# Kernel tuning notes

Hardware: AMD Instinct MI355X
Metric: run time of the kernel (lower is better)

## Reference

```python
import jax, jax.numpy as jnp
import numpy as np

CONF_THRESHOLD = 0.25
IOU_THRESHOLD = 0.5
MAX_OUT_DETS = 300
CELL_DIM = 640.0
PRE_NMS_TOPK = 4096  # fixed-size candidate set for jit-compatible NMS
N_ANCHORS = 134400   # 2560px input, strides 8/16/32
N_CLASSES = 80


def setup_inputs() -> dict:
    key = jax.random.key(0)
    preds = jax.random.uniform(key, (1, 4 + N_CLASSES, N_ANCHORS), dtype=jnp.float32)
    # scale the 4 box channels (xc, yc, w, h) to pixel range, keep class scores in [0,1]
    scale = jnp.concatenate([jnp.full((4,), CELL_DIM, jnp.float32),
                             jnp.ones((N_CLASSES,), jnp.float32)])
    preds = preds * scale[None, :, None]
    return {"yolo_preds": preds}


def _pairwise_iou(boxes):
    # boxes: [K, 4] in x1,y1,x2,y2 — torchvision-style IoU (no +1)
    area = (boxes[:, 2] - boxes[:, 0]) * (boxes[:, 3] - boxes[:, 1])
    lt = jnp.maximum(boxes[:, None, :2], boxes[None, :, :2])
    rb = jnp.minimum(boxes[:, None, 2:], boxes[None, :, 2:])
    wh = jnp.clip(rb - lt, 0.0)
    inter = wh[..., 0] * wh[..., 1]
    union = area[:, None] + area[None, :] - inter
    return inter / (union + 1e-9)


def _forward(yolo_preds):
    p = yolo_preds[0]                      # [4+C, A] (batch index [0] as in original)
    cls = p[4:4 + N_CLASSES]               # [C, A]
    scores = jnp.max(cls, axis=0)          # [A]
    classes = jnp.argmax(cls, axis=0)      # [A] int

    # box decode: note torch float `//` is floor division
    xc, yc, w, h = p[0], p[1], p[2], p[3]
    hw = jnp.floor(w / 2.0)
    hh = jnp.floor(h / 2.0)
    boxes = jnp.stack([xc - hw, yc - hh, xc + hw, yc + hh], axis=1)  # [A, 4]

    # confidence threshold mask (jit-compatible: mask to -inf instead of dynamic filter)
    masked = jnp.where(scores >= CONF_THRESHOLD, scores, -jnp.inf)

    # fixed-size pre-NMS top-k candidate selection (sorted descending)
    cand_scores, idx = jax.lax.top_k(masked, PRE_NMS_TOPK)   # [K]
    cand_boxes = boxes[idx]                                   # [K, 4]
    cand_classes = classes[idx]                               # [K]
    cand_valid = jnp.isfinite(cand_scores)                    # padding / below-threshold

    # greedy class-agnostic NMS (original uses plain torchvision.ops.nms)
    iou = _pairwise_iou(cand_boxes)                           # [K, K]
    k_idx = jnp.arange(PRE_NMS_TOPK)
    suppress = (iou > IOU_THRESHOLD) & (k_idx[None, :] > k_idx[:, None])  # j>i upper tri

    def body(i, keep):
        sup = suppress[i] & keep[i]
        return keep & ~sup

    keep = jax.lax.fori_loop(0, PRE_NMS_TOPK, body, cand_valid)

    # final top-k among survivors
    kept_scores = jnp.where(keep, cand_scores, -jnp.inf)
    final_scores, fidx = jax.lax.top_k(kept_scores, MAX_OUT_DETS)
    final_valid = jnp.isfinite(final_scores)
    final_boxes = jnp.where(final_valid[:, None], cand_boxes[fidx] / CELL_DIM, 0.0)
    final_classes = jnp.where(final_valid, cand_classes[fidx], 0)
    final_scores = jnp.where(final_valid, final_scores, 0.0)

    # tie-break quirk from the original: if the last two scores are ~equal,
    # zero out every score within 1e-5 of the last one
    tie = jnp.abs(final_scores[-1] - final_scores[-2]) < 1e-6
    factor = jnp.where(tie,
                       (final_scores - final_scores[-1] > 1e-5).astype(final_scores.dtype),
                       jnp.ones((), final_scores.dtype))
    final_scores = final_scores * factor

    count = jnp.sum(final_scores > 1e-5)
    return final_boxes, final_scores, final_classes, count


def reference(yolo_preds):
    return _forward(yolo_preds)
```

## Files before the change

kernel.cpp:

```cpp
#include <hip/hip_runtime.h>
#include <math.h>

#define N_ANCH 134400
#define N_CLS  80
#define TOPK   4096
#define MAX_OUT 300
#define TIECAP 16384

#define SARR_OFF   0u
#define GHIST_OFF  537600u
#define STATE_OFF  541696u
#define CNT_OFF    541704u
#define TIECNT_OFF 541708u
#define CLS8_OFF   541712u
#define TIEBUF_OFF 676112u
#define CANDK_OFF  741648u
#define CBOX_OFF   774416u
#define CSCORE_OFF 839952u
#define CCLS_OFF   856336u
#define SUP_OFF    872720u
#define WS_NEEDED  2969872u
#define MEMSET_OFF 537600u
#define MEMSET_LEN 4112u

static __device__ __forceinline__ unsigned int ord_f32(float f) {
  unsigned int u = __float_as_uint(f);
  return (u & 0x80000000u) ? ~u : (u | 0x80000000u);
}
static __device__ __forceinline__ float unord_f32(unsigned int o) {
  unsigned int u = (o & 0x80000000u) ? (o ^ 0x80000000u) : ~o;
  return __uint_as_float(u);
}

__global__ __launch_bounds__(256) void k_keys(const float* __restrict__ p,
                                              unsigned int* __restrict__ sarr,
                                              unsigned char* __restrict__ cls8,
                                              unsigned int* __restrict__ ghist) {
  __shared__ unsigned int h[256];
  int tid = threadIdx.x;
  h[tid] = 0u;
  __syncthreads();
  int i = blockIdx.x * 256 + tid;
  float best = p[4 * N_ANCH + i];
  int cls = 0;
  for (int c = 1; c < N_CLS; ++c) {
    float v = p[(4 + c) * N_ANCH + i];
    if (v > best) { best = v; cls = c; }
  }
  float m = (best >= 0.25f) ? best : -INFINITY;
  unsigned int s = ord_f32(m);
  sarr[i] = s;
  cls8[i] = (unsigned char)cls;
  atomicAdd(&h[s >> 24], 1u);
  __syncthreads();
  if (h[tid]) atomicAdd(&ghist[tid], h[tid]);
}

template <int PASS>
__global__ __launch_bounds__(256) void k_hist(const unsigned int* __restrict__ sarr,
                                              const unsigned int* __restrict__ state,
                                              unsigned int* __restrict__ ghist) {
  __shared__ unsigned int h[256];
  int tid = threadIdx.x;
  h[tid] = 0u;
  __syncthreads();
  int i = blockIdx.x * 256 + tid;
  unsigned int s = sarr[i];
  const int sh = 24 - 8 * PASS;
  if ((s >> (sh + 8)) == state[0])
    atomicAdd(&h[(s >> sh) & 255u], 1u);
  __syncthreads();
  if (h[tid]) atomicAdd(&ghist[PASS * 256 + tid], h[tid]);
}

template <int PASS>
__global__ __launch_bounds__(256) void k_scan(const unsigned int* __restrict__ ghist,
                                              unsigned int* __restrict__ state) {
  __shared__ unsigned int h[256];
  int tid = threadIdx.x;
  h[tid] = ghist[PASS * 256 + tid];
  __syncthreads();
  if (tid == 0) {
    unsigned int r    = (PASS == 0) ? (unsigned)TOPK : state[1];
    unsigned int pref = (PASS == 0) ? 0u : state[0];
    unsigned int cum = 0u;
    for (int b = 255; b >= 0; --b) {
      unsigned int c = h[b];
      if (cum + c >= r) { state[0] = (pref << 8) | (unsigned int)b; state[1] = r - cum; break; }
      cum += c;
    }
  }
}

__global__ void k_gathertie(const unsigned int* __restrict__ sarr,
                            const unsigned int* __restrict__ state,
                            unsigned int* __restrict__ counter,
                            unsigned int* __restrict__ tiecnt,
                            unsigned int* __restrict__ tiebuf,
                            unsigned long long* __restrict__ candk) {
  int i = blockIdx.x * 256 + threadIdx.x;
  unsigned int s = sarr[i];
  unsigned int S = state[0];
  if (s > S) {
    unsigned int pos = atomicAdd(counter, 1u);
    if (pos < TOPK)
      candk[pos] = ((unsigned long long)s << 32) |
                   (unsigned long long)(~(unsigned int)i);
  } else if (s == S) {
    unsigned int tp = atomicAdd(tiecnt, 1u);
    if (tp < TIECAP) tiebuf[tp] = (unsigned int)i;
  }
}

__global__ __launch_bounds__(256) void k_tieappend(const unsigned int* __restrict__ state,
                                                   const unsigned int* __restrict__ counter,
                                                   const unsigned int* __restrict__ tiecnt,
                                                   const unsigned int* __restrict__ tiebuf,
                                                   unsigned long long* __restrict__ candk) {
  __shared__ unsigned int buf[TIECAP];
  unsigned int n = *tiecnt; if (n > TIECAP) n = TIECAP;
  unsigned int rf = state[1];
  unsigned int cnt0 = *counter;
  unsigned long long Shi = ((unsigned long long)state[0]) << 32;
  for (unsigned int t = threadIdx.x; t < n; t += 256) buf[t] = tiebuf[t];
  __syncthreads();
  for (unsigned int t = threadIdx.x; t < n; t += 256) {
    unsigned int v = buf[t], r = 0u;
    for (unsigned int j = 0; j < n; ++j) r += (buf[j] < v) ? 1u : 0u;
    if (r < rf) candk[cnt0 + r] = Shi | (unsigned long long)(~v);
  }
}

__global__ __launch_bounds__(1024) void k_sort(unsigned long long* __restrict__ candk) {
  __shared__ unsigned long long s[TOPK];
  for (int i = threadIdx.x; i < TOPK; i += 1024) s[i] = candk[i];
  __syncthreads();
  for (int k = 2; k <= TOPK; k <<= 1) {
    for (int j = k >> 1; j > 0; j >>= 1) {
      for (int i = threadIdx.x; i < TOPK; i += 1024) {
        int ixj = i ^ j;
        if (ixj > i) {
          bool up = ((i & k) == 0);
          unsigned long long a = s[i], b = s[ixj];
          bool sw = up ? (a < b) : (a > b);
          if (sw) { s[i] = b; s[ixj] = a; }
        }
      }
      __syncthreads();
    }
  }
  for (int i = threadIdx.x; i < TOPK; i += 1024) candk[i] = s[i];
}

__global__ void k_fill(const float* __restrict__ p,
                       const unsigned char* __restrict__ cls8,
                       const unsigned long long* __restrict__ candk,
                       float4* __restrict__ cbox,
                       float* __restrict__ cscore,
                       int* __restrict__ ccls) {
  int c = blockIdx.x * blockDim.x + threadIdx.x;
  if (c >= TOPK) return;
  unsigned long long k = candk[c];
  float score = unord_f32((unsigned int)(k >> 32));
  int idx = (int)(~(unsigned int)(k & 0xFFFFFFFFull));
  float xc = p[idx];
  float yc = p[N_ANCH + idx];
  float w  = p[2 * N_ANCH + idx];
  float h  = p[3 * N_ANCH + idx];
  float hw = floorf(w * 0.5f), hh = floorf(h * 0.5f);
  cbox[c] = make_float4(xc - hw, yc - hh, xc + hw, yc + hh);
  cscore[c] = score;
  ccls[c]   = (int)cls8[idx];
}

__global__ void k_iou(const float4* __restrict__ cbox, unsigned long long* __restrict__ sup) {
  int g = blockIdx.x * blockDim.x + threadIdx.x;
  int row = g >> 6, word = g & 63;
  float4 bi = cbox[row];
  float ai = (bi.z - bi.x) * (bi.w - bi.y);
  unsigned long long m = 0ull;
  int j0 = word << 6;
  if (j0 + 63 > row) {
    for (int b = 0; b < 64; ++b) {
      int j = j0 + b;
      if (j <= row) continue;
      float4 bj = cbox[j];
      float aj = (bj.z - bj.x) * (bj.w - bj.y);
      float ltx = fmaxf(bi.x, bj.x), lty = fmaxf(bi.y, bj.y);
      float rbx = fminf(bi.z, bj.z), rby = fminf(bi.w, bj.w);
      float ww = fmaxf(rbx - ltx, 0.0f), hh = fmaxf(rby - lty, 0.0f);
      float inter = ww * hh;
      float uni = ai + aj - inter;
      float iou = inter / (uni + 1e-9f);
      if (iou > 0.5f) m |= (1ull << b);
    }
  }
  sup[g] = m;
}

__global__ __launch_bounds__(256) void k_nms_out(const float4* __restrict__ cbox,
                                                 const float* __restrict__ cscore,
                                                 const int* __restrict__ ccls,
                                                 const unsigned long long* __restrict__ sup,
                                                 float* __restrict__ out) {
  __shared__ unsigned long long skeep[64];
  __shared__ unsigned long long s_keptl;
  __shared__ int s_list[MAX_OUT];
  __shared__ float s_fs[MAX_OUT];
  __shared__ int s_K;
  __shared__ int s_cnt;
  int tid = threadIdx.x;
  int lane = tid & 63, wave = tid >> 6;

  for (int r = 0; r < 16; ++r) {
    float sc = cscore[r * 256 + tid];
    unsigned long long m = __ballot(sc >= 0.25f);
    if (lane == 0) skeep[r * 4 + wave] = m;
  }
  if (tid == 0) { s_K = 0; s_cnt = 0; }
  __syncthreads();

  for (int chunk = 0; chunk < 64; ++chunk) {
    unsigned long long cur0 = skeep[chunk];
    if (cur0 == 0ull) continue;
    unsigned long long rowv[16];
#pragma unroll
    for (int t = 0; t < 16; ++t)
      rowv[t] = sup[(unsigned)(chunk * 64 + wave * 16 + t) * 64 + lane];
    if (wave == 0) {
      unsigned long long diag = sup[(chunk * 64 + lane) * 64 + chunk];
      unsigned long long cur = cur0;
      unsigned long long keptl = 0ull;
      int n = s_K;
      while (cur) {
        int b = __builtin_ctzll(cur);
        if (lane == 0) s_list[n] = chunk * 64 + b;
        n++;
        keptl |= (1ull << b);
        if (n == MAX_OUT) break;
        unsigned long long mb = __shfl(diag, b);
        cur &= ~mb;
        cur = (b == 63) ? 0ull : (cur & (~0ull << (b + 1)));
      }
      if (lane == 0) { s_K = n; s_keptl = keptl; }
    }
    __syncthreads();
    if (s_K >= MAX_OUT) break;
    unsigned long long keptl = s_keptl;
    unsigned long long acc = 0ull;
#pragma unroll
    for (int t = 0; t < 16; ++t) {
      unsigned long long sel = 0ull - ((keptl >> (wave * 16 + t)) & 1ull);
      acc |= rowv[t] & sel;
    }
    if (acc) atomicAnd(&skeep[lane], ~acc);
    __syncthreads();
  }
  __syncthreads();

  int K = s_K;
  for (int r = tid; r < MAX_OUT; r += 256)
    s_fs[r] = (r < K) ? cscore[s_list[r]] : 0.0f;
  __syncthreads();

  float slast = s_fs[MAX_OUT - 1], sprev = s_fs[MAX_OUT - 2];
  bool tie = fabsf(slast - sprev) < 1e-6f;
  int local = 0;
  for (int r = tid; r < MAX_OUT; r += 256) {
    float fs = s_fs[r];
    float factor = tie ? ((fs - slast > 1e-5f) ? 1.0f : 0.0f) : 1.0f;
    float so = fs * factor;
    out[4 * MAX_OUT + r] = so;
    if (so > 1e-5f) local++;
    if (r < K) {
      int c = s_list[r];
      float4 b = cbox[c];
      out[4 * r + 0] = b.x / 640.0f;
      out[4 * r + 1] = b.y / 640.0f;
      out[4 * r + 2] = b.z / 640.0f;
      out[4 * r + 3] = b.w / 640.0f;
      out[5 * MAX_OUT + r] = (float)ccls[c];
    } else {
      out[4 * r + 0] = 0.0f; out[4 * r + 1] = 0.0f;
      out[4 * r + 2] = 0.0f; out[4 * r + 3] = 0.0f;
      out[5 * MAX_OUT + r] = 0.0f;
    }
  }
  if (local) atomicAdd(&s_cnt, local);
  __syncthreads();
  if (tid == 0) out[6 * MAX_OUT] = (float)s_cnt;
}

extern "C" void kernel_launch(void* const* d_in, const int* in_sizes, int n_in,
                              void* d_out, int out_size, void* d_ws, size_t ws_size,
                              hipStream_t stream) {
  const float* p = (const float*)d_in[0];
  float* out = (float*)d_out;
  char* ws = (char*)d_ws;

  if (ws_size < (size_t)WS_NEEDED) return;

  unsigned int* sarr    = (unsigned int*)(ws + SARR_OFF);
  unsigned int* ghist   = (unsigned int*)(ws + GHIST_OFF);
  unsigned int* state   = (unsigned int*)(ws + STATE_OFF);
  unsigned int* counter = (unsigned int*)(ws + CNT_OFF);
  unsigned int* tiecnt  = (unsigned int*)(ws + TIECNT_OFF);
  unsigned char* cls8   = (unsigned char*)(ws + CLS8_OFF);
  unsigned int* tiebuf  = (unsigned int*)(ws + TIEBUF_OFF);
  unsigned long long* candk = (unsigned long long*)(ws + CANDK_OFF);
  float4* cbox              = (float4*)(ws + CBOX_OFF);
  float* cscore             = (float*)(ws + CSCORE_OFF);
  int* ccls                 = (int*)(ws + CCLS_OFF);
  unsigned long long* sup   = (unsigned long long*)(ws + SUP_OFF);

  const int NB = N_ANCH / 256;

  hipMemsetAsync(ws + MEMSET_OFF, 0, MEMSET_LEN, stream);
  k_keys<<<NB, 256, 0, stream>>>(p, sarr, cls8, ghist);
  k_scan<0><<<1, 256, 0, stream>>>(ghist, state);
  k_hist<1><<<NB, 256, 0, stream>>>(sarr, state, ghist);
  k_scan<1><<<1, 256, 0, stream>>>(ghist, state);
  k_hist<2><<<NB, 256, 0, stream>>>(sarr, state, ghist);
  k_scan<2><<<1, 256, 0, stream>>>(ghist, state);
  k_hist<3><<<NB, 256, 0, stream>>>(sarr, state, ghist);
  k_scan<3><<<1, 256, 0, stream>>>(ghist, state);
  k_gathertie<<<NB, 256, 0, stream>>>(sarr, state, counter, tiecnt, tiebuf, candk);
  k_tieappend<<<1, 256, 0, stream>>>(state, counter, tiecnt, tiebuf, candk);
  k_sort<<<1, 1024, 0, stream>>>(candk);
  k_fill<<<TOPK / 256, 256, 0, stream>>>(p, cls8, candk, cbox, cscore, ccls);
  k_iou<<<(TOPK * 64) / 256, 256, 0, stream>>>(cbox, sup);
  k_nms_out<<<1, 256, 0, stream>>>(cbox, cscore, ccls, sup, out);
}
```

Baseline: 310.2 us.

## Replace single-block bitonic sort with parallel rank-counting scatter fused into fill

Removes the one-block bitonic sort of the 4096 candidate keys and the separate fill kernel. A new kernel runs across 16 blocks. Each block loads all keys into shared memory, each thread counts how many keys are larger than its own to get its sorted rank, then decodes the box and scatters it to that rank. This swaps the serial-latency sort with many barriers for O(K^2) parallel comparisons spread over more CUs, and saves one launch. It relies on the keys being unique (the index is in the low bits) so the ranks form a permutation.

```diff
diff --git a/kernel.cpp b/kernel.cpp
--- a/kernel.cpp
+++ b/kernel.cpp
@@ -131,46 +131,31 @@
   }
 }
 
-__global__ __launch_bounds__(1024) void k_sort(unsigned long long* __restrict__ candk) {
-  __shared__ unsigned long long s[TOPK];
-  for (int i = threadIdx.x; i < TOPK; i += 1024) s[i] = candk[i];
-  __syncthreads();
-  for (int k = 2; k <= TOPK; k <<= 1) {
-    for (int j = k >> 1; j > 0; j >>= 1) {
-      for (int i = threadIdx.x; i < TOPK; i += 1024) {
-        int ixj = i ^ j;
-        if (ixj > i) {
-          bool up = ((i & k) == 0);
-          unsigned long long a = s[i], b = s[ixj];
-          bool sw = up ? (a < b) : (a > b);
-          if (sw) { s[i] = b; s[ixj] = a; }
-        }
-      }
-      __syncthreads();
-    }
-  }
-  for (int i = threadIdx.x; i < TOPK; i += 1024) candk[i] = s[i];
-}
-
-__global__ void k_fill(const float* __restrict__ p,
-                       const unsigned char* __restrict__ cls8,
-                       const unsigned long long* __restrict__ candk,
-                       float4* __restrict__ cbox,
-                       float* __restrict__ cscore,
-                       int* __restrict__ ccls) {
-  int c = blockIdx.x * blockDim.x + threadIdx.x;
-  if (c >= TOPK) return;
-  unsigned long long k = candk[c];
-  float score = unord_f32((unsigned int)(k >> 32));
-  int idx = (int)(~(unsigned int)(k & 0xFFFFFFFFull));
+__global__ __launch_bounds__(256) void k_rankfill(const float* __restrict__ p,
+                                                  const unsigned char* __restrict__ cls8,
+                                                  const unsigned long long* __restrict__ candk,
+                                                  float4* __restrict__ cbox,
+                                                  float* __restrict__ cscore,
+                                                  int* __restrict__ ccls) {
+  __shared__ unsigned long long keys[TOPK];
+  int tid = threadIdx.x;
+  for (int i = tid; i < TOPK; i += 256) keys[i] = candk[i];
+  __syncthreads();
+  int c = blockIdx.x * 256 + tid;
+  unsigned long long mine = keys[c];
+  int cnt = 0;
+#pragma unroll 8
+  for (int j = 0; j < TOPK; ++j) cnt += (keys[j] > mine) ? 1 : 0;
+  float score = unord_f32((unsigned int)(mine >> 32));
+  int idx = (int)(~(unsigned int)(mine & 0xFFFFFFFFull));
   float xc = p[idx];
   float yc = p[N_ANCH + idx];
   float w  = p[2 * N_ANCH + idx];
   float h  = p[3 * N_ANCH + idx];
   float hw = floorf(w * 0.5f), hh = floorf(h * 0.5f);
-  cbox[c] = make_float4(xc - hw, yc - hh, xc + hw, yc + hh);
-  cscore[c] = score;
-  ccls[c]   = (int)cls8[idx];
+  cbox[cnt] = make_float4(xc - hw, yc - hh, xc + hw, yc + hh);
+  cscore[cnt] = score;
+  ccls[cnt]   = (int)cls8[idx];
 }
 
 __global__ void k_iou(const float4* __restrict__ cbox, unsigned long long* __restrict__ sup) {
@@ -326,8 +311,7 @@
   k_scan<3><<<1, 256, 0, stream>>>(ghist, state);
   k_gathertie<<<NB, 256, 0, stream>>>(sarr, state, counter, tiecnt, tiebuf, candk);
   k_tieappend<<<1, 256, 0, stream>>>(state, counter, tiecnt, tiebuf, candk);
-  k_sort<<<1, 1024, 0, stream>>>(candk);
-  k_fill<<<TOPK / 256, 256, 0, stream>>>(p, cls8, candk, cbox, cscore, ccls);
+  k_rankfill<<<TOPK / 256, 256, 0, stream>>>(p, cls8, candk, cbox, cscore, ccls);
   k_iou<<<(TOPK * 64) / 256, 256, 0, stream>>>(cbox, sup);
   k_nms_out<<<1, 256, 0, stream>>>(cbox, cscore, ccls, sup, out);
 }
```

Measured after the change: 302.8 us. -2.4%, faster.
